# Performance work log

Hardware: AMD Instinct MI355X
Metric: run time of the kernel (lower is better)

Reference implementation:

```python
import jax, jax.numpy as jnp
import numpy as np


def conv1d(x, w, b, pad):
    # x: (B, Cin, T), w: (Cout, Cin, K), b: (Cout,)
    y = jax.lax.conv_general_dilated(x, w, window_strides=(1,), padding=[(pad, pad)],
                                     dimension_numbers=('NCH', 'OIH', 'NCH'))
    return y + b[None, :, None]


def setup_inputs() -> dict:
    key = jax.random.key(0)
    ks = jax.random.split(key, 12)
    B, Cm, T1, Ct, T2, Ca = 8, 80, 800, 512, 200, 80
    queries = jax.random.normal(ks[0], (B, Cm, T1), dtype=jnp.float32)
    keys = jax.random.normal(ks[1], (B, Ct, T2), dtype=jnp.float32)
    query_lens = jnp.full((B,), T1, dtype=jnp.int32)
    key_lens = jax.random.randint(ks[2], (B,), T2 // 2, T2 + 1)
    # mask True where key position is padding (>= key_len): (B, T2, 1)
    mask = (jnp.arange(T2)[None, :] >= key_lens[:, None])[:, :, None]
    attn_prior = jax.random.uniform(ks[3], (B, T1, T2), dtype=jnp.float32) + 0.1
    # key_proj: Conv1d(512->1024, k=3, pad=1) + ReLU + Conv1d(1024->80, k=1)
    kp_w1 = jax.random.normal(ks[4], (2 * Ct, Ct, 3), jnp.float32) * 0.02
    kp_b1 = jnp.zeros((2 * Ct,), jnp.float32)
    kp_w2 = jax.random.normal(ks[5], (Ca, 2 * Ct, 1), jnp.float32) * 0.02
    kp_b2 = jnp.zeros((Ca,), jnp.float32)
    # query_proj (3xconv): Conv1d(80->160,k3)+ReLU+Conv1d(160->80,k1)+ReLU+Conv1d(80->80,k1)
    qp_w1 = jax.random.normal(ks[6], (2 * Cm, Cm, 3), jnp.float32) * 0.05
    qp_b1 = jnp.zeros((2 * Cm,), jnp.float32)
    qp_w2 = jax.random.normal(ks[7], (Cm, 2 * Cm, 1), jnp.float32) * 0.05
    qp_b2 = jnp.zeros((Cm,), jnp.float32)
    qp_w3 = jax.random.normal(ks[8], (Ca, Cm, 1), jnp.float32) * 0.05
    qp_b3 = jnp.zeros((Ca,), jnp.float32)
    return {"queries": queries, "keys": keys, "query_lens": query_lens, "mask": mask,
            "attn_prior": attn_prior, "kp_w1": kp_w1, "kp_b1": kp_b1, "kp_w2": kp_w2,
            "kp_b2": kp_b2, "qp_w1": qp_w1, "qp_b1": qp_b1, "qp_w2": qp_w2,
            "qp_b2": qp_b2, "qp_w3": qp_w3, "qp_b3": qp_b3}


def reference(queries, keys, query_lens, mask, attn_prior,
              kp_w1, kp_b1, kp_w2, kp_b2,
              qp_w1, qp_b1, qp_w2, qp_b2, qp_w3, qp_b3):
    # key projection: (B, Ct, T2) -> (B, Ca, T2)
    ke = conv1d(keys, kp_w1, kp_b1, pad=1)
    ke = jax.nn.relu(ke)
    ke = conv1d(ke, kp_w2, kp_b2, pad=0)
    # query projection ('3xconv'): (B, Cm, T1) -> (B, Ca, T1)
    qe = conv1d(queries, qp_w1, qp_b1, pad=1)
    qe = jax.nn.relu(qe)
    qe = conv1d(qe, qp_w2, qp_b2, pad=0)
    qe = jax.nn.relu(qe)
    qe = conv1d(qe, qp_w3, qp_b3, pad=0)
    # broadcasted squared L2 distance: (B, Ca, T1, T2) -> reduce C -> (B, 1, T1, T2)
    diff2 = (qe[:, :, :, None] - ke[:, :, None, :]) ** 2
    attn = -0.0005 * jnp.sum(diff2, axis=1, keepdims=True)
    # prior in log domain
    attn = jax.nn.log_softmax(attn, axis=3) + jnp.log(attn_prior[:, None] + 1e-8)
    attn_logprob = attn
    # mask (B, T2, 1) -> (B, 1, 1, T2)
    m = jnp.transpose(mask, (0, 2, 1))[:, :, None, :]
    attn = jnp.where(m, -jnp.inf, attn)
    attn = jax.nn.softmax(attn, axis=3)
    return (attn, attn_logprob)
```

## Files before the change

kernel.cpp:

```cpp
#include <hip/hip_runtime.h>
#include <hip/hip_bf16.h>
#include <math.h>

#define B_  8
#define CM  80
#define T1_ 800
#define CT  512
#define T2_ 200
#define CA  80

using bf16 = __hip_bfloat16;
typedef __attribute__((ext_vector_type(8))) short bf16x8;
typedef __attribute__((ext_vector_type(4))) float f32x4;

#define LDSW 56
#define LDSW2 72

__device__ __forceinline__ float load_sel(const void* p, long idx, int isf32) {
  if (isf32) return ((const float*)p)[idx];
  return __bfloat162float(((const bf16*)p)[idx]);
}

__device__ __forceinline__ unsigned short f2bf(float x) {
  bf16 h = __float2bfloat16(x);
  return *reinterpret_cast<unsigned short*>(&h);
}

__device__ __forceinline__ int detect_f32(const unsigned short* q) {
  __shared__ int s_f;
  const int tid = threadIdx.x;
  if (tid < 64) {
    unsigned short u = q[2 * tid];
    int e = (u >> 7) & 0xFF;
    unsigned long long bal = __ballot(e < 100 || e > 154);
    if (tid == 0) s_f = (__popcll(bal) >= 16) ? 1 : 0;
  }
  __syncthreads();
  return s_f;
}

__device__ void task_cvt_t(const void* X, bf16* XT, int f, int C, int T,
                           int id2, int tilesT, float* smem, int tid) {
  const int per_b = tilesT * ((C + 31) >> 5);
  const int b = id2 / per_b;
  const int r = id2 - b * per_b;
  const int ct = r / tilesT, tt = r - ct * tilesT;
  const int c0 = ct * 32, t0 = tt * 32;
  const int tx = tid & 31, trow = tid >> 5;
#pragma unroll
  for (int p = 0; p < 4; ++p) {
    const int cr = trow + 8 * p;
    if (c0 + cr < C && t0 + tx < T)
      smem[cr * 33 + tx] = load_sel(X, ((long)b * C + c0 + cr) * T + t0 + tx, f);
  }
  __syncthreads();
#pragma unroll
  for (int p = 0; p < 4; ++p) {
    const int tr = trow + 8 * p;
    if (t0 + tr < T && c0 + tx < C)
      XT[((long)b * T + t0 + tr) * C + c0 + tx] =
          __float2bfloat16(smem[tx * 33 + tr]);
  }
}

__device__ void task_wt3(const void* W, bf16* WT, int f, int Co, int Ci,
                         int id2, int tid) {
  const int i = id2 * 256 + tid;
  if (i >= Co * Ci) return;
  const int co = i / Ci, ci = i - co * Ci;
#pragma unroll
  for (int dk = 0; dk < 3; ++dk)
    WT[((long)dk * Co + co) * Ci + ci] =
        __float2bfloat16(load_sel(W, ((long)co * Ci + ci) * 3 + dk, f));
}

__device__ void task_cvt(const void* W, bf16* O, int f, int n, int id2, int tid) {
  const int i = id2 * 256 + tid;
  if (i < n) O[i] = __float2bfloat16(load_sel(W, i, f));
}

__global__ __launch_bounds__(256) void k_prep(
    const void* __restrict__ queries, const void* __restrict__ keys,
    const void* __restrict__ mask,
    const void* __restrict__ kp_w1, const void* __restrict__ kp_b1,
    const void* __restrict__ kp_w2, const void* __restrict__ kp_b2,
    const void* __restrict__ qp_w1, const void* __restrict__ qp_b1,
    const void* __restrict__ qp_w2, const void* __restrict__ qp_b2,
    const void* __restrict__ qp_w3, const void* __restrict__ qp_b3,
    bf16* __restrict__ keysT, bf16* __restrict__ queriesT,
    bf16* __restrict__ w1T, bf16* __restrict__ qw1T,
    bf16* __restrict__ kw2c, bf16* __restrict__ qw2c, bf16* __restrict__ qw3c,
    float* __restrict__ biasf, float* __restrict__ mf) {
  __shared__ float smem[32 * 33];
  const int tid = threadIdx.x;
  const int f = detect_f32((const unsigned short*)queries);
  int id = blockIdx.x;

  if (id < 896) { task_cvt_t(keys, keysT, f, CT, T2_, id, 7, smem, tid); return; }
  id -= 896;
  if (id < 600) { task_cvt_t(queries, queriesT, f, CM, T1_, id, 25, smem, tid); return; }
  id -= 600;
  if (id < 2048) { task_wt3(kp_w1, w1T, f, 1024, CT, id, tid); return; }
  id -= 2048;
  if (id < 50) { task_wt3(qp_w1, qw1T, f, 160, CM, id, tid); return; }
  id -= 50;
  if (id < 320) { task_cvt(kp_w2, kw2c, f, 80 * 1024, id, tid); return; }
  id -= 320;
  if (id < 50) { task_cvt(qp_w2, qw2c, f, 80 * 160, id, tid); return; }
  id -= 50;
  if (id < 25) { task_cvt(qp_w3, qw3c, f, 80 * 80, id, tid); return; }
  id -= 25;

  if (id == 0) {
    for (int i = tid; i < 1424; i += 256) {
      float v;
      if (i < 1024)      v = load_sel(kp_b1, i, f);
      else if (i < 1104) v = load_sel(kp_b2, i - 1024, f);
      else if (i < 1264) v = load_sel(qp_b1, i - 1104, f);
      else if (i < 1344) v = load_sel(qp_b2, i - 1264, f);
      else               v = load_sel(qp_b3, i - 1344, f);
      biasf[i] = v;
    }
    return;
  }

  {
    int* s_fmt = (int*)smem;
    const int nmask = B_ * T2_;
    if (tid == 0) s_fmt[0] = 1;
    __syncthreads();
    const unsigned int* wi = (const unsigned int*)mask;
    const int nw = nmask / 4;
    int pri = 0;
    for (int i = tid; i < nw; i += 256) {
      unsigned int w = wi[i];
      if (w == 0u || w == 1u) continue;
      if (w == 0x3F803F80u || w == 0x00003F80u) { pri = max(pri, 2); continue; }
      if (w == 0x3F800000u) continue;
      unsigned int b0 = w & 0xFFu, b1 = (w >> 8) & 0xFFu,
                   b2 = (w >> 16) & 0xFFu, b3 = (w >> 24) & 0xFFu;
      if (b0 <= 1u && b1 <= 1u && b2 <= 1u && b3 <= 1u) pri = max(pri, 3);
      else pri = max(pri, 2);
    }
    if (pri) atomicMax(&s_fmt[0], pri);
    __syncthreads();
    const int fmt = s_fmt[0];
    for (int i = tid; i < nmask; i += 256) {
      int m;
      if (fmt == 3)      m = ((const unsigned char*)mask)[i] != 0;
      else if (fmt == 2) m = ((const unsigned short*)mask)[i] != 0;
      else               m = (wi[i] != 0u);
      mf[i] = (float)m;
    }
  }
}

__device__ void conv_tile(
    const bf16* __restrict__ XT, const bf16* __restrict__ WT,
    const float* __restrict__ bias, void* __restrict__ Y,
    int Cin, int Cout, int T, int KW, int pad, int relu, int outmode,
    int m0, int n0, short* As, short* Bs) {
  const int K = Cin * KW;
  const int tid = threadIdx.x;
  const int wave = tid >> 6;
  const int lane = tid & 63;

  const int row = tid >> 2;
  const int koff = (tid & 3) * 8;
  const int n = n0 + row;
  const int bb = n / T;
  const int t = n - bb * T;

  const int wm = (wave >> 1) * 32;
  const int wn = (wave & 1) * 32;
  const int fm = lane & 15;
  const int quad = lane >> 4;

  f32x4 acc[2][2] = {};

  const short* ap0 = As + (wm + fm) * LDSW + quad * 8;
  const short* bp0 = Bs + (wn + fm) * LDSW + quad * 8;

  for (int k0 = 0; k0 < K; k0 += 32) {
    {
      const int k = k0 + koff;
      const int m = m0 + row;
      uint4 v = {0u, 0u, 0u, 0u};
      if (m < Cout && k < K) {
        const int dk = k / Cin;
        const int ci = k - dk * Cin;
        v = *(const uint4*)(WT + ((long)dk * Cout + m) * Cin + ci);
      }
      *(uint4*)(As + row * LDSW + koff) = v;
    }
    {
      const int k = k0 + koff;
      uint4 v = {0u, 0u, 0u, 0u};
      if (k < K) {
        const int dk = k / Cin;
        const int ci = k - dk * Cin;
        const int tt = t + dk - pad;
        if (tt >= 0 && tt < T)
          v = *(const uint4*)(XT + ((long)bb * T + tt) * Cin + ci);
      }
      *(uint4*)(Bs + row * LDSW + koff) = v;
    }
    __syncthreads();
    {
      bf16x8 a0 = *(const bf16x8*)(ap0);
      bf16x8 a1 = *(const bf16x8*)(ap0 + 16 * LDSW);
      bf16x8 b0 = *(const bf16x8*)(bp0);
      bf16x8 b1 = *(const bf16x8*)(bp0 + 16 * LDSW);
      acc[0][0] = __builtin_amdgcn_mfma_f32_16x16x32_bf16(a0, b0, acc[0][0], 0, 0, 0);
      acc[0][1] = __builtin_amdgcn_mfma_f32_16x16x32_bf16(a0, b1, acc[0][1], 0, 0, 0);
      acc[1][0] = __builtin_amdgcn_mfma_f32_16x16x32_bf16(a1, b0, acc[1][0], 0, 0, 0);
      acc[1][1] = __builtin_amdgcn_mfma_f32_16x16x32_bf16(a1, b1, acc[1][1], 0, 0, 0);
    }
    __syncthreads();
  }

#pragma unroll
  for (int mi = 0; mi < 2; ++mi) {
    const int mrow = m0 + wm + mi * 16 + quad * 4;
    if (mrow >= Cout) continue;
    float bi[4];
#pragma unroll
    for (int r = 0; r < 4; ++r) bi[r] = bias[mrow + r];
#pragma unroll
    for (int ni = 0; ni < 2; ++ni) {
      const int ncol = n0 + wn + ni * 16 + fm;
      const long base = (long)ncol * Cout + mrow;
      float o[4];
#pragma unroll
      for (int r = 0; r < 4; ++r) {
        float v = acc[mi][ni][r] + bi[r];
        if (relu) v = fmaxf(v, 0.f);
        o[r] = v;
      }
      if (outmode == 0) {
        ushort4 u;
        u.x = f2bf(o[0]); u.y = f2bf(o[1]); u.z = f2bf(o[2]); u.w = f2bf(o[3]);
        *(ushort4*)((bf16*)Y + base) = u;
      } else {
        *(float4*)((float*)Y + base) = make_float4(o[0], o[1], o[2], o[3]);
      }
    }
  }
}

__device__ void conv_tile64_k1(
    const bf16* __restrict__ XT, const bf16* __restrict__ WT,
    const float* __restrict__ bias, bf16* __restrict__ Y,
    int m0, int n0, short* As, short* Bs) {
  const int Cin = CT, Cout = 1024, T = T2_, K = 1536;
  const int tid = threadIdx.x;
  const int wave = tid >> 6;
  const int lane = tid & 63;

  const int row = tid >> 2;
  const int koff = (tid & 3) * 8;
  const int n = n0 + row;
  const int bb = n / T;
  const int t = n - bb * T;

  const int wm = (wave >> 1) * 32;
  const int wn = (wave & 1) * 32;
  const int fm = lane & 15;
  const int quad = lane >> 4;

  f32x4 acc[2][2] = {};

  const short* ap0 = As + (wm + fm) * LDSW2 + quad * 8;
  const short* bp0 = Bs + (wn + fm) * LDSW2 + quad * 8;

  for (int k0 = 0; k0 < K; k0 += 64) {
#pragma unroll
    for (int h = 0; h < 2; ++h) {
      const int k = k0 + h * 32 + koff;
      const int dk = k / Cin;
      const int ci = k - dk * Cin;
      {
        uint4 v = *(const uint4*)(WT + ((long)dk * Cout + m0 + row) * Cin + ci);
        *(uint4*)(As + row * LDSW2 + h * 32 + koff) = v;
      }
      {
        const int tt = t + dk - 1;
        uint4 v = {0u, 0u, 0u, 0u};
        if (tt >= 0 && tt < T)
          v = *(const uint4*)(XT + ((long)bb * T + tt) * Cin + ci);
        *(uint4*)(Bs + row * LDSW2 + h * 32 + koff) = v;
      }
    }
    __syncthreads();
#pragma unroll
    for (int h = 0; h < 2; ++h) {
      bf16x8 a0 = *(const bf16x8*)(ap0 + h * 32);
      bf16x8 a1 = *(const bf16x8*)(ap0 + 16 * LDSW2 + h * 32);
      bf16x8 b0 = *(const bf16x8*)(bp0 + h * 32);
      bf16x8 b1 = *(const bf16x8*)(bp0 + 16 * LDSW2 + h * 32);
      acc[0][0] = __builtin_amdgcn_mfma_f32_16x16x32_bf16(a0, b0, acc[0][0], 0, 0, 0);
      acc[0][1] = __builtin_amdgcn_mfma_f32_16x16x32_bf16(a0, b1, acc[0][1], 0, 0, 0);
      acc[1][0] = __builtin_amdgcn_mfma_f32_16x16x32_bf16(a1, b0, acc[1][0], 0, 0, 0);
      acc[1][1] = __builtin_amdgcn_mfma_f32_16x16x32_bf16(a1, b1, acc[1][1], 0, 0, 0);
    }
    __syncthreads();
  }

#pragma unroll
  for (int mi = 0; mi < 2; ++mi) {
    const int mrow = m0 + wm + mi * 16 + quad * 4;
    float bi[4];
#pragma unroll
    for (int r = 0; r < 4; ++r) bi[r] = bias[mrow + r];
#pragma unroll
    for (int ni = 0; ni < 2; ++ni) {
      const int ncol = n0 + wn + ni * 16 + fm;
      const long base = (long)ncol * Cout + mrow;
      ushort4 u;
      u.x = f2bf(fmaxf(acc[mi][ni][0] + bi[0], 0.f));
      u.y = f2bf(fmaxf(acc[mi][ni][1] + bi[1], 0.f));
      u.z = f2bf(fmaxf(acc[mi][ni][2] + bi[2], 0.f));
      u.w = f2bf(fmaxf(acc[mi][ni][3] + bi[3], 0.f));
      *(ushort4*)(Y + base) = u;
    }
  }
}

__global__ __launch_bounds__(256) void k_conv1(
    const bf16* __restrict__ keysT, const bf16* __restrict__ w1T,
    const float* __restrict__ b_k1, bf16* __restrict__ ke1T,
    const bf16* __restrict__ queriesT, const bf16* __restrict__ qw1T,
    const float* __restrict__ b_q1, bf16* __restrict__ qe1T) {
  __shared__ __align__(16) short sA[64 * LDSW2];
  __shared__ __align__(16) short sB[64 * LDSW2];
  int j = blockIdx.x;
  if (j < 400) {
    conv_tile64_k1(keysT, w1T, b_k1, ke1T, (j / 25) * 64, (j % 25) * 64, sA, sB);
  } else {
    j -= 400;
    conv_tile(queriesT, qw1T, b_q1, qe1T, CM, 160, T1_, 3, 1, 1, 0,
              (j / 100) * 64, (j % 100) * 64, sA, sB);
  }
}

__global__ __launch_bounds__(256) void k_conv2(
    const bf16* __restrict__ ke1T, const bf16* __restrict__ kw2c,
    const float* __restrict__ b_k2, float* __restrict__ keT,
    const bf16* __restrict__ qe1T, const bf16* __restrict__ qw2c,
    const float* __restrict__ b_q2, bf16* __restrict__ qe2T) {
  __shared__ __align__(16) short sA[64 * LDSW];
  __shared__ __align__(16) short sB[64 * LDSW];
  int j = blockIdx.x;
  if (j < 50) {
    conv_tile(ke1T, kw2c, b_k2, keT, 1024, CA, T2_, 1, 0, 0, 1,
              (j / 25) * 64, (j % 25) * 64, sA, sB);
  } else {
    j -= 50;
    conv_tile(qe1T, qw2c, b_q2, qe2T, 160, CM, T1_, 1, 0, 1, 0,
              (j / 100) * 64, (j % 100) * 64, sA, sB);
  }
}

__global__ __launch_bounds__(256) void k_conv3(
    const bf16* __restrict__ qe2T, const bf16* __restrict__ qw3c,
    const float* __restrict__ b_q3, float* __restrict__ qeT) {
  __shared__ __align__(16) short sA[64 * LDSW];
  __shared__ __align__(16) short sB[64 * LDSW];
  const int j = blockIdx.x;
  conv_tile(qe2T, qw3c, b_q3, qeT, CM, CA, T1_, 1, 0, 0, 1,
            (j / 100) * 64, (j % 100) * 64, sA, sB);
}

__global__ __launch_bounds__(256) void k_dist(
    const float* __restrict__ qeT, const float* __restrict__ keT,
    const void* __restrict__ prior, const float* __restrict__ mf,
    void* __restrict__ out, const unsigned short* __restrict__ qprobe) {
  __shared__ float sq[4 * CA];
  __shared__ float red[8];
  const int f = detect_f32(qprobe);
  const int b = blockIdx.y;
  const int t1base = blockIdx.x * 4;
  const int tid = threadIdx.x;

  for (int i = tid; i < 4 * CA; i += 256) {
    int u = i / CA, c = i - u * CA;
    sq[i] = qeT[((long)b * T1_ + t1base + u) * CA + c];
  }
  __syncthreads();

  const int t2 = tid;
  const bool valid = (t2 < T2_);
  float x[4] = {-INFINITY, -INFINITY, -INFINITY, -INFINITY};
  if (valid) {
    const float4* kb = (const float4*)(keT + ((long)b * T2_ + t2) * CA);
    float s[4] = {0.f, 0.f, 0.f, 0.f};
#pragma unroll 4
    for (int j = 0; j < CA / 4; ++j) {
      float4 kv = kb[j];
#pragma unroll
      for (int u = 0; u < 4; ++u) {
        float4 qv = ((const float4*)(sq + u * CA))[j];
        float d;
        d = qv.x - kv.x; s[u] = fmaf(d, d, s[u]);
        d = qv.y - kv.y; s[u] = fmaf(d, d, s[u]);
        d = qv.z - kv.z; s[u] = fmaf(d, d, s[u]);
        d = qv.w - kv.w; s[u] = fmaf(d, d, s[u]);
      }
    }
#pragma unroll
    for (int u = 0; u < 4; ++u) x[u] = -0.0005f * s[u];
  }

  const float mval = valid ? mf[b * T2_ + t2] : 0.f;
  const long N = (long)B_ * T1_ * T2_;

#pragma unroll
  for (int u = 0; u < 4; ++u) {
    const int t1 = t1base + u;
    const float xx = x[u];

    float m = xx;
#pragma unroll
    for (int o = 32; o > 0; o >>= 1) m = fmaxf(m, __shfl_down(m, o, 64));
    if ((tid & 63) == 0) red[tid >> 6] = m;
    __syncthreads();
    const float M1 = fmaxf(fmaxf(red[0], red[1]), fmaxf(red[2], red[3]));

    float e = (xx == -INFINITY) ? 0.f : expf(xx - M1);
    float ssum = e;
#pragma unroll
    for (int o = 32; o > 0; o >>= 1) ssum += __shfl_down(ssum, o, 64);
    if ((tid & 63) == 0) red[(tid >> 6) + 4] = ssum;
    __syncthreads();
    const float S1 = red[4] + red[5] + red[6] + red[7];
    const float logZ = logf(S1);

    const long oidx = ((long)b * T1_ + t1) * T2_ + t2;
    float lp = -INFINITY;
    if (valid) {
      float pr = load_sel(prior, oidx, f);
      lp = (xx - M1 - logZ) + logf(fmaxf(pr, 0.f) + 1e-8f);
      if (f) ((float*)out)[N + oidx] = lp;
      else   ((bf16*)out)[N + oidx] = __float2bfloat16(lp);
    }

    float xm = lp;
    if (valid && mval != 0.f) xm = -INFINITY;

    __syncthreads();
    float m2 = xm;
#pragma unroll
    for (int o = 32; o > 0; o >>= 1) m2 = fmaxf(m2, __shfl_down(m2, o, 64));
    if ((tid & 63) == 0) red[tid >> 6] = m2;
    __syncthreads();
    const float M2 = fmaxf(fmaxf(red[0], red[1]), fmaxf(red[2], red[3]));

    float e2 = (xm == -INFINITY) ? 0.f : expf(xm - M2);
    float s2 = e2;
#pragma unroll
    for (int o = 32; o > 0; o >>= 1) s2 += __shfl_down(s2, o, 64);
    if ((tid & 63) == 0) red[(tid >> 6) + 4] = s2;
    __syncthreads();
    const float S2 = red[4] + red[5] + red[6] + red[7];

    if (valid) {
      float a = (S2 > 0.f) ? (e2 / S2) : 0.f;
      if (f) ((float*)out)[oidx] = a;
      else   ((bf16*)out)[oidx] = __float2bfloat16(a);
    }
    __syncthreads();
  }
}

extern "C" void kernel_launch(void* const* d_in, const int* in_sizes, int n_in,
                              void* d_out, int out_size, void* d_ws, size_t ws_size,
                              hipStream_t stream) {
  const void* queries = d_in[0];
  const void* keys    = d_in[1];
  const void* mask    = d_in[3];
  const void* prior   = d_in[4];
  const void* kp_w1 = d_in[5];
  const void* kp_b1 = d_in[6];
  const void* kp_w2 = d_in[7];
  const void* kp_b2 = d_in[8];
  const void* qp_w1 = d_in[9];
  const void* qp_b1 = d_in[10];
  const void* qp_w2 = d_in[11];
  const void* qp_b2 = d_in[12];
  const void* qp_w3 = d_in[13];
  const void* qp_b3 = d_in[14];

  float* keT   = (float*)d_ws;
  float* qeT   = keT + 128000;
  float* mf    = qeT + 512000;
  float* biasf = mf + 1600;
  bf16* keysT    = (bf16*)(biasf + 1440);
  bf16* queriesT = keysT + 819200;
  bf16* w1T      = queriesT + 512000;
  bf16* qw1T     = w1T + 1572864;
  bf16* kw2c     = qw1T + 38400;
  bf16* qw2c     = kw2c + 81920;
  bf16* qw3c     = qw2c + 12800;
  bf16* ke1T     = qw3c + 6400;
  bf16* qe1T     = ke1T + 1638400;
  bf16* qe2T     = qe1T + 1024000;

  float* b_k1 = biasf;
  float* b_k2 = biasf + 1024;
  float* b_q1 = biasf + 1104;
  float* b_q2 = biasf + 1264;
  float* b_q3 = biasf + 1344;

  k_prep<<<3991, 256, 0, stream>>>(
      queries, keys, mask,
      kp_w1, kp_b1, kp_w2, kp_b2,
      qp_w1, qp_b1, qp_w2, qp_b2, qp_w3, qp_b3,
      keysT, queriesT, w1T, qw1T, kw2c, qw2c, qw3c, biasf, mf);

  k_conv1<<<700, 256, 0, stream>>>(keysT, w1T, b_k1, ke1T,
                                   queriesT, qw1T, b_q1, qe1T);

  k_conv2<<<250, 256, 0, stream>>>(ke1T, kw2c, b_k2, keT,
                                   qe1T, qw2c, b_q2, qe2T);

  k_conv3<<<200, 256, 0, stream>>>(qe2T, qw3c, b_q3, qeT);

  k_dist<<<dim3(200, B_), 256, 0, stream>>>(
      qeT, keT, prior, mf, d_out, (const unsigned short*)queries);
}
```

Measured before the change: 172.2 us.

## Fuse query conv2+conv3, vectorize weight prep, batch softmax reductions

Merges the second and third query-projection convolutions into one MFMA tile that keeps the intermediate activation in LDS, removing one kernel launch and the qe2T global round trip. Weight conversion tasks in the prep kernel now handle four elements per thread with vector loads and stores, which cuts the prep grid size. The distance kernel's four per-row softmax reductions are interleaved so each reduction phase needs one barrier instead of four, trading that for more registers and shuffles in flight. The fused conv tile uses a larger shared buffer, which may lower occupancy.

```diff
diff --git a/kernel.cpp b/kernel.cpp
--- a/kernel.cpp
+++ b/kernel.cpp
@@ -15,6 +15,8 @@
 
 #define LDSW 56
 #define LDSW2 72
+#define LDSW3 168
+#define LDSW4 104
 
 __device__ __forceinline__ float load_sel(const void* p, long idx, int isf32) {
   if (isf32) return ((const float*)p)[idx];
@@ -63,20 +65,44 @@
   }
 }
 
-__device__ void task_wt3(const void* W, bf16* WT, int f, int Co, int Ci,
-                         int id2, int tid) {
+__device__ void task_wt3v(const void* W, bf16* WT, int f, int Co, int Ci,
+                          int id2, int tid) {
   const int i = id2 * 256 + tid;
-  if (i >= Co * Ci) return;
-  const int co = i / Ci, ci = i - co * Ci;
-#pragma unroll
-  for (int dk = 0; dk < 3; ++dk)
-    WT[((long)dk * Co + co) * Ci + ci] =
-        __float2bfloat16(load_sel(W, ((long)co * Ci + ci) * 3 + dk, f));
-}
-
-__device__ void task_cvt(const void* W, bf16* O, int f, int n, int id2, int tid) {
-  const int i = id2 * 256 + tid;
-  if (i < n) O[i] = __float2bfloat16(load_sel(W, i, f));
+  const int g4 = Ci >> 2;
+  if (i >= Co * g4) return;
+  const int co = i / g4, ci = (i - co * g4) * 4;
+  const long sbase = ((long)co * Ci + ci) * 3;
+  float w[12];
+  if (f) {
+    const float4* s = (const float4*)((const float*)W + sbase);
+    float4 f0 = s[0], f1 = s[1], f2 = s[2];
+    w[0]=f0.x; w[1]=f0.y; w[2]=f0.z; w[3]=f0.w; w[4]=f1.x; w[5]=f1.y;
+    w[6]=f1.z; w[7]=f1.w; w[8]=f2.x; w[9]=f2.y; w[10]=f2.z; w[11]=f2.w;
+  } else {
+#pragma unroll
+    for (int j = 0; j < 12; ++j) w[j] = load_sel(W, sbase + j, 0);
+  }
+#pragma unroll
+  for (int dk = 0; dk < 3; ++dk) {
+    ushort4 u;
+    u.x = f2bf(w[0 * 3 + dk]); u.y = f2bf(w[1 * 3 + dk]);
+    u.z = f2bf(w[2 * 3 + dk]); u.w = f2bf(w[3 * 3 + dk]);
+    *(ushort4*)(WT + ((long)dk * Co + co) * Ci + ci) = u;
+  }
+}
+
+__device__ void task_cvtv(const void* W, bf16* O, int f, int n, int id2, int tid) {
+  const int i = (id2 * 256 + tid) * 4;
+  if (i >= n) return;
+  ushort4 u;
+  if (f) {
+    float4 v = *(const float4*)((const float*)W + i);
+    u.x = f2bf(v.x); u.y = f2bf(v.y); u.z = f2bf(v.z); u.w = f2bf(v.w);
+  } else {
+    u.x = f2bf(load_sel(W, i, 0));     u.y = f2bf(load_sel(W, i + 1, 0));
+    u.z = f2bf(load_sel(W, i + 2, 0)); u.w = f2bf(load_sel(W, i + 3, 0));
+  }
+  *(ushort4*)(O + i) = u;
 }
 
 __global__ __launch_bounds__(256) void k_prep(
@@ -100,16 +126,16 @@
   id -= 896;
   if (id < 600) { task_cvt_t(queries, queriesT, f, CM, T1_, id, 25, smem, tid); return; }
   id -= 600;
-  if (id < 2048) { task_wt3(kp_w1, w1T, f, 1024, CT, id, tid); return; }
-  id -= 2048;
-  if (id < 50) { task_wt3(qp_w1, qw1T, f, 160, CM, id, tid); return; }
-  id -= 50;
-  if (id < 320) { task_cvt(kp_w2, kw2c, f, 80 * 1024, id, tid); return; }
-  id -= 320;
-  if (id < 50) { task_cvt(qp_w2, qw2c, f, 80 * 160, id, tid); return; }
-  id -= 50;
-  if (id < 25) { task_cvt(qp_w3, qw3c, f, 80 * 80, id, tid); return; }
-  id -= 25;
+  if (id < 512) { task_wt3v(kp_w1, w1T, f, 1024, CT, id, tid); return; }
+  id -= 512;
+  if (id < 13) { task_wt3v(qp_w1, qw1T, f, 160, CM, id, tid); return; }
+  id -= 13;
+  if (id < 80) { task_cvtv(kp_w2, kw2c, f, 80 * 1024, id, tid); return; }
+  id -= 80;
+  if (id < 13) { task_cvtv(qp_w2, qw2c, f, 80 * 160, id, tid); return; }
+  id -= 13;
+  if (id < 7) { task_cvtv(qp_w3, qw3c, f, 80 * 80, id, tid); return; }
+  id -= 7;
 
   if (id == 0) {
     for (int i = tid; i < 1424; i += 256) {
@@ -343,32 +369,110 @@
   }
 }
 
-__global__ __launch_bounds__(256) void k_conv2(
+__device__ void conv23_tile(
+    const bf16* __restrict__ qe1T, const bf16* __restrict__ qw2c,
+    const float* __restrict__ b_q2, const bf16* __restrict__ qw3c,
+    const float* __restrict__ b_q3, float* __restrict__ qeT,
+    int n0, short* smem) {
+  short* sIn = smem;
+  short* sW2 = smem + 64 * LDSW3;
+  short* sC  = smem;
+  short* sW3 = smem + 64 * LDSW3;
+  const int tid = threadIdx.x;
+  const int wave = tid >> 6;
+  const int lane = tid & 63;
+  const int fm = lane & 15;
+  const int quad = lane >> 4;
+
+#pragma unroll
+  for (int c = tid; c < 1280; c += 256) {
+    const int row = c / 20, kc = (c - row * 20) * 8;
+    uint4 v = *(const uint4*)(qe1T + (long)(n0 + row) * 160 + kc);
+    *(uint4*)(sIn + row * LDSW3 + kc) = v;
+  }
+  for (int c = tid; c < 1600; c += 256) {
+    const int row = c / 20, kc = (c - row * 20) * 8;
+    uint4 v = *(const uint4*)(qw2c + (long)row * 160 + kc);
+    *(uint4*)(sW2 + row * LDSW3 + kc) = v;
+  }
+  __syncthreads();
+
+  f32x4 acc1[5] = {};
+#pragma unroll
+  for (int ks = 0; ks < 5; ++ks) {
+    bf16x8 b = *(const bf16x8*)(sIn + (16 * wave + fm) * LDSW3 + ks * 32 + quad * 8);
+#pragma unroll
+    for (int mt = 0; mt < 5; ++mt) {
+      bf16x8 a = *(const bf16x8*)(sW2 + (16 * mt + fm) * LDSW3 + ks * 32 + quad * 8);
+      acc1[mt] = __builtin_amdgcn_mfma_f32_16x16x32_bf16(a, b, acc1[mt], 0, 0, 0);
+    }
+  }
+  __syncthreads();
+
+#pragma unroll
+  for (int mt = 0; mt < 5; ++mt) {
+    const int ch = 16 * mt + quad * 4;
+    const float4 b2 = *(const float4*)(b_q2 + ch);
+    ushort4 u;
+    u.x = f2bf(fmaxf(acc1[mt][0] + b2.x, 0.f));
+    u.y = f2bf(fmaxf(acc1[mt][1] + b2.y, 0.f));
+    u.z = f2bf(fmaxf(acc1[mt][2] + b2.z, 0.f));
+    u.w = f2bf(fmaxf(acc1[mt][3] + b2.w, 0.f));
+    *(ushort4*)(sC + (16 * wave + fm) * LDSW4 + ch) = u;
+  }
+  if (tid < 128) {
+    const int row = tid >> 1, off = 80 + (tid & 1) * 8;
+    uint4 z = {0u, 0u, 0u, 0u};
+    *(uint4*)(sC + row * LDSW4 + off) = z;
+  }
+  for (int c = tid; c < 800; c += 256) {
+    const int row = c / 10, kc = (c - row * 10) * 8;
+    uint4 v = *(const uint4*)(qw3c + (long)row * 80 + kc);
+    *(uint4*)(sW3 + row * LDSW4 + kc) = v;
+  }
+  if (tid < 160) {
+    const int row = tid >> 1, off = 80 + (tid & 1) * 8;
+    uint4 z = {0u, 0u, 0u, 0u};
+    *(uint4*)(sW3 + row * LDSW4 + off) = z;
+  }
+  __syncthreads();
+
+  f32x4 acc2[5] = {};
+#pragma unroll
+  for (int ks = 0; ks < 3; ++ks) {
+    bf16x8 b = *(const bf16x8*)(sC + (16 * wave + fm) * LDSW4 + ks * 32 + quad * 8);
+#pragma unroll
+    for (int mt = 0; mt < 5; ++mt) {
+      bf16x8 a = *(const bf16x8*)(sW3 + (16 * mt + fm) * LDSW4 + ks * 32 + quad * 8);
+      acc2[mt] = __builtin_amdgcn_mfma_f32_16x16x32_bf16(a, b, acc2[mt], 0, 0, 0);
+    }
+  }
+
+  const int pos = n0 + 16 * wave + fm;
+#pragma unroll
+  for (int mt = 0; mt < 5; ++mt) {
+    const int ch = 16 * mt + quad * 4;
+    const float4 b3 = *(const float4*)(b_q3 + ch);
+    float4 o = make_float4(acc2[mt][0] + b3.x, acc2[mt][1] + b3.y,
+                           acc2[mt][2] + b3.z, acc2[mt][3] + b3.w);
+    *(float4*)(qeT + (long)pos * CA + ch) = o;
+  }
+}
+
+__global__ __launch_bounds__(256) void k_conv2f(
     const bf16* __restrict__ ke1T, const bf16* __restrict__ kw2c,
     const float* __restrict__ b_k2, float* __restrict__ keT,
     const bf16* __restrict__ qe1T, const bf16* __restrict__ qw2c,
-    const float* __restrict__ b_q2, bf16* __restrict__ qe2T) {
-  __shared__ __align__(16) short sA[64 * LDSW];
-  __shared__ __align__(16) short sB[64 * LDSW];
+    const float* __restrict__ b_q2, const bf16* __restrict__ qw3c,
+    const float* __restrict__ b_q3, float* __restrict__ qeT) {
+  __shared__ __align__(16) short smem[64 * LDSW3 + 80 * LDSW3];
   int j = blockIdx.x;
   if (j < 50) {
     conv_tile(ke1T, kw2c, b_k2, keT, 1024, CA, T2_, 1, 0, 0, 1,
-              (j / 25) * 64, (j % 25) * 64, sA, sB);
+              (j / 25) * 64, (j % 25) * 64, smem, smem + 64 * LDSW);
   } else {
-    j -= 50;
-    conv_tile(qe1T, qw2c, b_q2, qe2T, 160, CM, T1_, 1, 0, 1, 0,
-              (j / 100) * 64, (j % 100) * 64, sA, sB);
-  }
-}
-
-__global__ __launch_bounds__(256) void k_conv3(
-    const bf16* __restrict__ qe2T, const bf16* __restrict__ qw3c,
-    const float* __restrict__ b_q3, float* __restrict__ qeT) {
-  __shared__ __align__(16) short sA[64 * LDSW];
-  __shared__ __align__(16) short sB[64 * LDSW];
-  const int j = blockIdx.x;
-  conv_tile(qe2T, qw3c, b_q3, qeT, CM, CA, T1_, 1, 0, 0, 1,
-            (j / 100) * 64, (j % 100) * 64, sA, sB);
+    conv23_tile(qe1T, qw2c, b_q2, qw3c, b_q3, qeT, (j - 50) * 64, smem);
+  }
 }
 
 __global__ __launch_bounds__(256) void k_dist(
@@ -376,11 +480,12 @@
     const void* __restrict__ prior, const float* __restrict__ mf,
     void* __restrict__ out, const unsigned short* __restrict__ qprobe) {
   __shared__ float sq[4 * CA];
-  __shared__ float red[8];
+  __shared__ float redA[16], redB[16], redC[16], redD[16];
   const int f = detect_f32(qprobe);
   const int b = blockIdx.y;
   const int t1base = blockIdx.x * 4;
   const int tid = threadIdx.x;
+  const int wid = tid >> 6;
 
   for (int i = tid; i < 4 * CA; i += 256) {
     int u = i / CA, c = i - u * CA;
@@ -414,61 +519,91 @@
   const float mval = valid ? mf[b * T2_ + t2] : 0.f;
   const long N = (long)B_ * T1_ * T2_;
 
+  float m[4] = {x[0], x[1], x[2], x[3]};
+#pragma unroll
+  for (int o = 32; o > 0; o >>= 1)
+#pragma unroll
+    for (int u = 0; u < 4; ++u) m[u] = fmaxf(m[u], __shfl_down(m[u], o, 64));
+  if ((tid & 63) == 0)
+#pragma unroll
+    for (int u = 0; u < 4; ++u) redA[wid * 4 + u] = m[u];
+  __syncthreads();
+  float M1[4];
+#pragma unroll
+  for (int u = 0; u < 4; ++u)
+    M1[u] = fmaxf(fmaxf(redA[u], redA[4 + u]), fmaxf(redA[8 + u], redA[12 + u]));
+
+  float e[4], s1[4];
 #pragma unroll
   for (int u = 0; u < 4; ++u) {
-    const int t1 = t1base + u;
-    const float xx = x[u];
-
-    float m = xx;
-#pragma unroll
-    for (int o = 32; o > 0; o >>= 1) m = fmaxf(m, __shfl_down(m, o, 64));
-    if ((tid & 63) == 0) red[tid >> 6] = m;
-    __syncthreads();
-    const float M1 = fmaxf(fmaxf(red[0], red[1]), fmaxf(red[2], red[3]));
-
-    float e = (xx == -INFINITY) ? 0.f : expf(xx - M1);
-    float ssum = e;
-#pragma unroll
-    for (int o = 32; o > 0; o >>= 1) ssum += __shfl_down(ssum, o, 64);
-    if ((tid & 63) == 0) red[(tid >> 6) + 4] = ssum;
-    __syncthreads();
-    const float S1 = red[4] + red[5] + red[6] + red[7];
+    e[u] = (x[u] == -INFINITY) ? 0.f : expf(x[u] - M1[u]);
+    s1[u] = e[u];
+  }
+#pragma unroll
+  for (int o = 32; o > 0; o >>= 1)
+#pragma unroll
+    for (int u = 0; u < 4; ++u) s1[u] += __shfl_down(s1[u], o, 64);
+  if ((tid & 63) == 0)
+#pragma unroll
+    for (int u = 0; u < 4; ++u) redB[wid * 4 + u] = s1[u];
+  __syncthreads();
+  float lp[4];
+#pragma unroll
+  for (int u = 0; u < 4; ++u) {
+    const float S1 = redB[u] + redB[4 + u] + redB[8 + u] + redB[12 + u];
     const float logZ = logf(S1);
-
-    const long oidx = ((long)b * T1_ + t1) * T2_ + t2;
-    float lp = -INFINITY;
+    lp[u] = -INFINITY;
     if (valid) {
+      const long oidx = ((long)b * T1_ + t1base + u) * T2_ + t2;
       float pr = load_sel(prior, oidx, f);
-      lp = (xx - M1 - logZ) + logf(fmaxf(pr, 0.f) + 1e-8f);
-      if (f) ((float*)out)[N + oidx] = lp;
-      else   ((bf16*)out)[N + oidx] = __float2bfloat16(lp);
-    }
-
-    float xm = lp;
-    if (valid && mval != 0.f) xm = -INFINITY;
-
-    __syncthreads();
-    float m2 = xm;
-#pragma unroll
-    for (int o = 32; o > 0; o >>= 1) m2 = fmaxf(m2, __shfl_down(m2, o, 64));
-    if ((tid & 63) == 0) red[tid >> 6] = m2;
-    __syncthreads();
-    const float M2 = fmaxf(fmaxf(red[0], red[1]), fmaxf(red[2], red[3]));
-
-    float e2 = (xm == -INFINITY) ? 0.f : expf(xm - M2);
-    float s2 = e2;
-#pragma unroll
-    for (int o = 32; o > 0; o >>= 1) s2 += __shfl_down(s2, o, 64);
-    if ((tid & 63) == 0) red[(tid >> 6) + 4] = s2;
-    __syncthreads();
-    const float S2 = red[4] + red[5] + red[6] + red[7];
-
+      lp[u] = (x[u] - M1[u] - logZ) + logf(fmaxf(pr, 0.f) + 1e-8f);
+      if (f) ((float*)out)[N + oidx] = lp[u];
+      else   ((bf16*)out)[N + oidx] = __float2bfloat16(lp[u]);
+    }
+  }
+
+  float xm[4], m2[4];
+#pragma unroll
+  for (int u = 0; u < 4; ++u) {
+    xm[u] = (valid && mval != 0.f) ? -INFINITY : lp[u];
+    m2[u] = xm[u];
+  }
+#pragma unroll
+  for (int o = 32; o > 0; o >>= 1)
+#pragma unroll
+    for (int u = 0; u < 4; ++u) m2[u] = fmaxf(m2[u], __shfl_down(m2[u], o, 64));
+  if ((tid & 63) == 0)
+#pragma unroll
+    for (int u = 0; u < 4; ++u) redC[wid * 4 + u] = m2[u];
+  __syncthreads();
+  float M2[4];
+#pragma unroll
+  for (int u = 0; u < 4; ++u)
+    M2[u] = fmaxf(fmaxf(redC[u], redC[4 + u]), fmaxf(redC[8 + u], redC[12 + u]));
+
+  float e2[4], s2[4];
+#pragma unroll
+  for (int u = 0; u < 4; ++u) {
+    e2[u] = (xm[u] == -INFINITY) ? 0.f : expf(xm[u] - M2[u]);
+    s2[u] = e2[u];
+  }
+#pragma unroll
+  for (int o = 32; o > 0; o >>= 1)
+#pragma unroll
+    for (int u = 0; u < 4; ++u) s2[u] += __shfl_down(s2[u], o, 64);
+  if ((tid & 63) == 0)
+#pragma unroll
+    for (int u = 0; u < 4; ++u) redD[wid * 4 + u] = s2[u];
+  __syncthreads();
+#pragma unroll
+  for (int u = 0; u < 4; ++u) {
+    const float S2 = redD[u] + redD[4 + u] + redD[8 + u] + redD[12 + u];
     if (valid) {
-      float a = (S2 > 0.f) ? (e2 / S2) : 0.f;
+      float a = (S2 > 0.f) ? (e2[u] / S2) : 0.f;
+      const long oidx = ((long)b * T1_ + t1base + u) * T2_ + t2;
       if (f) ((float*)out)[oidx] = a;
       else   ((bf16*)out)[oidx] = __float2bfloat16(a);
     }
-    __syncthreads();
   }
 }
 
@@ -503,7 +638,6 @@
   bf16* qw3c     = qw2c + 12800;
   bf16* ke1T     = qw3c + 6400;
   bf16* qe1T     = ke1T + 1638400;
-  bf16* qe2T     = qe1T + 1024000;
 
   float* b_k1 = biasf;
   float* b_k2 = biasf + 1024;
@@ -511,7 +645,7 @@
   float* b_q2 = biasf + 1264;
   float* b_q3 = biasf + 1344;
 
-  k_prep<<<3991, 256, 0, stream>>>(
+  k_prep<<<2123, 256, 0, stream>>>(
       queries, keys, mask,
       kp_w1, kp_b1, kp_w2, kp_b2,
       qp_w1, qp_b1, qp_w2, qp_b2, qp_w3, qp_b3,
@@ -520,10 +654,8 @@
   k_conv1<<<700, 256, 0, stream>>>(keysT, w1T, b_k1, ke1T,
                                    queriesT, qw1T, b_q1, qe1T);
 
-  k_conv2<<<250, 256, 0, stream>>>(ke1T, kw2c, b_k2, keT,
-                                   qe1T, qw2c, b_q2, qe2T);
-
-  k_conv3<<<200, 256, 0, stream>>>(qe2T, qw3c, b_q3, qeT);
+  k_conv2f<<<150, 256, 0, stream>>>(ke1T, kw2c, b_k2, keT,
+                                    qe1T, qw2c, b_q2, qw3c, b_q3, qeT);
 
   k_dist<<<dim3(200, B_), 256, 0, stream>>>(
       qeT, keT, prior, mf, d_out, (const unsigned short*)queries);
```

New measurement: 168.1 us. -2.4%, faster.
